# Optimization experiments

Measured on AMD Instinct MI355X. Metric: run time of the kernel, lower is better.

## Reference

```python
import jax, jax.numpy as jnp
import numpy as np

BATCH, SEQ, D_MODEL, D_STATE = 4, 2048, 512, 64
LN_EPS = 1e-5

def setup_inputs() -> dict:
    key = jax.random.key(0)
    ks = jax.random.split(key, 8)
    x = jax.random.normal(ks[0], (BATCH, SEQ, D_MODEL), jnp.float32)
    log_A_real = jax.random.normal(ks[1], (D_MODEL, D_STATE), jnp.float32)
    A_imag = jax.random.normal(ks[2], (D_MODEL, D_STATE), jnp.float32)
    B_param = jax.random.normal(ks[3], (D_MODEL, D_STATE, 2), jnp.float32) * 0.01
    C_param = jax.random.normal(ks[4], (D_MODEL, D_STATE, 2), jnp.float32) * 0.01
    D_param = jnp.ones((D_MODEL,), jnp.float32)
    W_out = jax.random.normal(ks[5], (D_MODEL, D_MODEL), jnp.float32) * (1.0 / np.sqrt(D_MODEL))
    b_out = jnp.zeros((D_MODEL,), jnp.float32)
    gamma = jnp.ones((D_MODEL,), jnp.float32)
    beta = jnp.zeros((D_MODEL,), jnp.float32)
    return dict(x=x, log_A_real=log_A_real, A_imag=A_imag, B_param=B_param,
                C_param=C_param, D_param=D_param, W_out=W_out, b_out=b_out,
                gamma=gamma, beta=beta)


def reference(x, log_A_real, A_imag, B_param, C_param, D_param, W_out, b_out, gamma, beta):
    Bn, L, d = x.shape
    # diagonal complex SSM parameters
    A = -jnp.exp(log_A_real) + 1j * A_imag                  # (d, s) complex, Re(A) < 0
    Bc = B_param[..., 0] + 1j * B_param[..., 1]              # (d, s)
    Cc = C_param[..., 0] + 1j * C_param[..., 1]              # (d, s)
    # kernel: K[d, l] = Re( sum_s conj(C) * exp(l*A) * B )
    powers = jnp.arange(L, dtype=jnp.float32)[:, None, None]  # (L,1,1)
    A_pow = jnp.exp(powers * A[None])                         # (L, d, s) complex
    CB = jnp.conj(Cc) * Bc                                    # (d, s)
    K = jnp.einsum('ds,lds->dl', CB, A_pow).real              # (d, L)
    # FFT convolution (matches torch flip + rfft conv + slice [L-1:2L-1])
    x_t = jnp.swapaxes(x, 1, 2)                               # (B, d, L)
    K_fl = jnp.flip(K, axis=-1)
    n = 2 * L
    Xf = jnp.fft.rfft(x_t, n=n, axis=-1)
    Kf = jnp.fft.rfft(K_fl, n=n, axis=-1)
    y = jnp.fft.irfft(Xf * Kf[None], n=n, axis=-1)[..., L - 1:2 * L - 1]
    y = y + D_param[None, :, None] * x_t                      # skip term D*x
    y = jnp.swapaxes(y, 1, 2)                                 # (B, L, d)
    y = y @ W_out.T + b_out                                   # out_proj (dropout p=0)
    z = y + x                                                 # residual
    mu = jnp.mean(z, axis=-1, keepdims=True)
    var = jnp.var(z, axis=-1, keepdims=True)
    return gamma * (z - mu) / jnp.sqrt(var + LN_EPS) + beta
```

## Files before the change

### kernel.cpp

```cpp
#include <hip/hip_runtime.h>
#include <hip/hip_bf16.h>
#include <stdint.h>
#include <stddef.h>

#define BATCH 4
#define SEQ   2048
#define DM    512
#define NST   64
#define LN_EPS 1e-5f
#define NCH   32
#define KDIM  192

typedef __attribute__((ext_vector_type(8))) short short8;
typedef __attribute__((ext_vector_type(4))) float f32x4;

__device__ __forceinline__ ushort f2bf(float f) {
    __hip_bfloat16 h = __float2bfloat16(f);
    return *(ushort*)&h;
}
__device__ __forceinline__ float bf2f(ushort u) {
    __hip_bfloat16 h = *(__hip_bfloat16*)&u;
    return __bfloat162float(h);
}

__global__ __launch_bounds__(256) void k_prep(
    const float* __restrict__ x, const float* __restrict__ W,
    __hip_bfloat16* __restrict__ xT, __hip_bfloat16* __restrict__ Wbf)
{
    __shared__ float smem[64][33];
    const int tid = threadIdx.x;
    const int bid = blockIdx.x;

    if (bid < 2048) {
        const int dt = bid & 15, lt = (bid >> 4) & 31, b = bid >> 9;
        const int l0 = lt * 64, d0 = dt * 32;
        const int dd = tid & 31, lr = tid >> 5;
        #pragma unroll
        for (int it = 0; it < 8; ++it) {
            int ll = it * 8 + lr;
            smem[ll][dd] = x[((size_t)b * SEQ + l0 + ll) * DM + d0 + dd];
        }
        __syncthreads();
        const int dw = tid >> 3, lg = (tid & 7) * 8;
        ushort pk[8];
        #pragma unroll
        for (int i = 0; i < 8; ++i) pk[i] = f2bf(smem[lg + i][dw]);
        *(short8*)&xT[((size_t)(d0 + dw) * BATCH + b) * SEQ + l0 + lg] = *(short8*)pk;
    } else {
        int i = (bid - 2048) * 256 + tid;
        if (i < DM * DM) Wbf[i] = __float2bfloat16(W[i]);
    }
}

__global__ __launch_bounds__(512) void k_ssm(
    const float* __restrict__ logA, const float* __restrict__ Aim,
    const float* __restrict__ Bp, const float* __restrict__ Cp,
    const __hip_bfloat16* __restrict__ xT, const float* __restrict__ Dp,
    __hip_bfloat16* __restrict__ yT)
{
    __shared__ short Zs[128 * 24 * 8];
    __shared__ __align__(16) char Rgn[128 * 129 * 4];
    __shared__ float Klds[64];
    __shared__ float2 e64s[64];
    short* Gs = (short*)Rgn;
    float (*Us)[129] = (float(*)[129])Rgn;
    short* Ms = (short*)Rgn;

    const int tid = threadIdx.x;
    const int d = blockIdx.x;
    const int w = tid >> 6, lane = tid & 63;
    const int q = lane >> 4, n = lane & 15;

    short8 xr[2];
    #pragma unroll
    for (int it = 0; it < 2; ++it) {
        int id = it * 512 + tid;
        int col = id >> 3, ck = id & 7;
        int bb = col >> 5, ch = col & 31;
        xr[it] = *(const short8*)&xT[((size_t)d * BATCH + bb) * SEQ + ch * 64 + ck * 8];
    }

    uint mca[8];
    {
        const int s = lane;
        const int i = d * NST + s;
        float aa  = expf(logA[i]);
        float wim = Aim[i];
        float mag = expf(-aa);
        float er = mag * cosf(wim), ei = mag * sinf(wim);
        float Br = Bp[2*i], Bi = Bp[2*i+1];
        float Cr = Cp[2*i], Ci = Cp[2*i+1];
        float CBr = Cr*Br + Ci*Bi;
        float CBi = Cr*Bi - Ci*Br;

        float e2r = er*er - ei*ei,   e2i = 2.f*er*ei;
        float e4r = e2r*e2r - e2i*e2i, e4i = 2.f*e2r*e2i;
        float e8r = e4r*e4r - e4i*e4i, e8i = 2.f*e4r*e4i;
        float ar, ai;
        if (w == 0)      { ar = 1.f;  ai = 0.f; }
        else if (w == 1) { ar = e8r;  ai = e8i; }
        else {
            float e16r = e8r*e8r - e8i*e8i, e16i = 2.f*e8r*e8i;
            if (w == 2)      { ar = e16r; ai = e16i; }
            else if (w == 3) { ar = e16r*e8r - e16i*e8i;  ai = e16r*e8i + e16i*e8r; }
            else {
                float e32r = e16r*e16r - e16i*e16i, e32i = 2.f*e16r*e16i;
                if (w == 4)      { ar = e32r; ai = e32i; }
                else if (w == 5) { ar = e32r*e8r - e32i*e8i;   ai = e32r*e8i + e32i*e8r; }
                else if (w == 6) { ar = e32r*e16r - e32i*e16i; ai = e32r*e16i + e32i*e16r; }
                else {
                    float e48r = e32r*e16r - e32i*e16i, e48i = e32r*e16i + e32i*e16r;
                    ar = e48r*e8r - e48i*e8i;  ai = e48r*e8i + e48i*e8r;
                }
            }
        }
        float prr = CBr*ar - CBi*ai;
        float pii = CBr*ai + CBi*ar;

        float kb[8];
        ushort gR[8], gI[8];
        #pragma unroll
        for (int tt = 0; tt < 8; ++tt) {
            kb[tt] = prr;
            gR[tt] = f2bf(prr);
            gI[tt] = f2bf(pii);
            float npr = er*prr - ei*pii, npi = er*pii + ei*prr;  prr = npr; pii = npi;
            float nar = er*ar - ei*ai,   nai = er*ai + ei*ar;    ar = nar; ai = nai;
            mca[tt] = (uint)f2bf(ar) | ((uint)f2bf(-ai) << 16);
        }
        if (w == 7) e64s[s] = make_float2(ar, ai);

        short8 v;
        int row = 2 * s;
        #pragma unroll
        for (int e = 0; e < 8; ++e) v[e] = (short)gR[e];
        { int cs = w ^ (row & 7); *(short8*)&Gs[(row * 8 + cs) * 8] = v; }
        row = 2 * s + 1;
        #pragma unroll
        for (int e = 0; e < 8; ++e) v[e] = (short)gI[e];
        { int cs = w ^ (row & 7); *(short8*)&Gs[(row * 8 + cs) * 8] = v; }

        #pragma unroll
        for (int tt = 0; tt < 8; ++tt) {
            float v2 = kb[tt];
            #pragma unroll
            for (int mask = 1; mask < 64; mask <<= 1) v2 += __shfl_xor(v2, mask);
            if (lane == 0) Klds[8 * w + tt] = v2;
        }
    }

    #pragma unroll
    for (int it = 0; it < 2; ++it) {
        int id = it * 512 + tid;
        int col = id >> 3, ck = id & 7;
        int cs = ck ^ (col & 7);
        *(short8*)&Zs[(col * 24 + cs) * 8] = xr[it];
    }
    __syncthreads();

    f32x4 acc1[8];
    {
        #pragma unroll
        for (int nf = 0; nf < 8; ++nf)
            #pragma unroll
            for (int k = 0; k < 4; ++k) acc1[nf][k] = 0.f;

        const int arow = w * 16 + n;
        #pragma unroll
        for (int kt = 0; kt < 2; ++kt) {
            int c = kt * 4 + q;
            int csa = c ^ (arow & 7);
            short8 af = *(const short8*)&Gs[(arow * 8 + csa) * 8];
            #pragma unroll
            for (int nf = 0; nf < 8; ++nf) {
                int col = nf * 16 + n;
                int csb = c ^ (col & 7);
                short8 bf = *(const short8*)&Zs[(col * 24 + csb) * 8];
                acc1[nf] = __builtin_amdgcn_mfma_f32_16x16x32_bf16(af, bf, acc1[nf], 0, 0, 0);
            }
        }
    }
    __syncthreads();

    {
        const int r0w = w * 16 + q * 4;
        #pragma unroll
        for (int nf = 0; nf < 8; ++nf) {
            int col = nf * 16 + n;
            #pragma unroll
            for (int r = 0; r < 4; ++r) Us[r0w + r][col] = acc1[nf][r];
        }
    }
    __syncthreads();

    if (tid < 256) {
        const int bb = tid >> 6, s = tid & 63;
        const int st = s >> 2, so = (s & 3) * 2;
        float2 a64 = e64s[s];
        const float er = a64.x, ei = a64.y;
        {
            int col = bb * 32 + 31;
            int c = 8 + st, cs = (c & ~7) | ((c & 7) ^ (col & 7));
            *(uint*)&Zs[(col * 24 + cs) * 8 + so] = 0u;
        }
        float gr = Us[2 * s][bb * 32 + 31], gi = Us[2 * s + 1][bb * 32 + 31];
        {
            int col = bb * 32 + 30;
            int c = 8 + st, cs = (c & ~7) | ((c & 7) ^ (col & 7));
            *(uint*)&Zs[(col * 24 + cs) * 8 + so] = (uint)f2bf(gr) | ((uint)f2bf(gi) << 16);
        }
        #pragma unroll 6
        for (int ch = 30; ch >= 1; --ch) {
            float ur = Us[2 * s][bb * 32 + ch], ui = Us[2 * s + 1][bb * 32 + ch];
            float nr = ur + er * gr - ei * gi;
            float ni = ui + er * gi + ei * gr;
            gr = nr; gi = ni;
            int col = bb * 32 + ch - 1;
            int c = 8 + st, cs = (c & ~7) | ((c & 7) ^ (col & 7));
            *(uint*)&Zs[(col * 24 + cs) * 8 + so] = (uint)f2bf(gr) | ((uint)f2bf(gi) << 16);
        }
    }
    __syncthreads();

    {
        {
            int id = tid;
            int row = id >> 3, c = id & 7;
            short8 v;
            #pragma unroll
            for (int e = 0; e < 8; ++e) {
                int col = c * 8 + e;
                float kv = (col >= row) ? Klds[col - row] : 0.f;
                v[e] = (short)f2bf(kv);
            }
            int cs = c ^ (row & 7);
            *(short8*)&Ms[(row * 24 + cs) * 8] = v;
        }
        const int s = lane;
        const int cc = 8 + (s >> 2);
        const int soff = 2 * (s & 3);
        #pragma unroll
        for (int tt = 0; tt < 8; ++tt) {
            int row = 63 - (8 * w + tt);
            int cs = (cc & ~7) | ((cc & 7) ^ (row & 7));
            *(uint*)&Ms[(row * 24 + cs) * 8 + soff] = mca[tt];
        }
    }
    __syncthreads();

    f32x4 acc[4];
    #pragma unroll
    for (int nf = 0; nf < 4; ++nf)
        #pragma unroll
        for (int k = 0; k < 4; ++k) acc[nf][k] = 0.f;

    const int arow = (w >> 1) * 16 + n;
    const int nfb  = (w & 1) * 4;
    #pragma unroll
    for (int kt = 0; kt < 6; ++kt) {
        int c = kt * 4 + q;
        int csa = (c & ~7) | ((c & 7) ^ (arow & 7));
        short8 af = *(const short8*)&Ms[(arow * 24 + csa) * 8];
        #pragma unroll
        for (int j = 0; j < 4; ++j) {
            int col = (nfb + j) * 16 + n;
            int csb = (c & ~7) | ((c & 7) ^ (col & 7));
            short8 bfr = *(const short8*)&Zs[(col * 24 + csb) * 8];
            acc[j] = __builtin_amdgcn_mfma_f32_16x16x32_bf16(af, bfr, acc[j], 0, 0, 0);
        }
    }

    const float Dd = Dp[d];
    const int i0 = (w >> 1) * 16 + q * 4;
    #pragma unroll
    for (int j = 0; j < 4; ++j) {
        int col = (nfb + j) * 16 + n;
        int bb = col >> 5, ch = col & 31;
        int cx = (i0 >> 3) ^ (col & 7);
        const ushort* zp = (const ushort*)&Zs[(col * 24 + cx) * 8 + (i0 & 7)];
        ushort o[4];
        #pragma unroll
        for (int r = 0; r < 4; ++r)
            o[r] = f2bf(acc[j][r] + Dd * bf2f(zp[r]));
        *(uint2*)&yT[((size_t)d * BATCH + bb) * SEQ + ch * 64 + i0] = *(uint2*)o;
    }
}

__global__ __launch_bounds__(512) void k_gemm_ln(
    const __hip_bfloat16* __restrict__ yT, const __hip_bfloat16* __restrict__ Wbf,
    const float* __restrict__ x, const float* __restrict__ bout,
    const float* __restrict__ gamma, const float* __restrict__ beta,
    float* __restrict__ out)
{
    __shared__ short Af[32][520];
    __shared__ short Bs[2][512][32];
    __shared__ float red[8][32][2];
    __shared__ float stats[32][2];

    const int tid  = threadIdx.x;
    const int w    = tid >> 6;
    const int lane = tid & 63;
    const int q    = lane >> 4;
    const int m    = lane & 15;
    const int r0   = blockIdx.x * 32;
    const int bq   = r0 >> 11;
    const int l0   = r0 & 2047;

    {
        const int kdb = tid >> 3, lg = (tid & 7) * 4;
        uint2 u[8];
        #pragma unroll
        for (int j = 0; j < 8; ++j)
            u[j] = *(const uint2*)&yT[((size_t)(j * 64 + kdb) * BATCH + bq) * SEQ + l0 + lg];
        #pragma unroll
        for (int j = 0; j < 8; ++j) {
            int kd = j * 64 + kdb;
            Af[lg + 0][kd] = (short)(u[j].x & 0xffff);
            Af[lg + 1][kd] = (short)(u[j].x >> 16);
            Af[lg + 2][kd] = (short)(u[j].y & 0xffff);
            Af[lg + 3][kd] = (short)(u[j].y >> 16);
        }
    }

    short8 nb0, nb1, nb2, nb3;
    const int ob = tid >> 2, jb = tid & 3;
    const int js = (jb ^ (ob & 3)) * 8;
    #define LOADB(k0) { \
        nb0 = *(const short8*)(Wbf + (size_t)(ob      ) * DM + (k0) + jb * 8); \
        nb1 = *(const short8*)(Wbf + (size_t)(ob + 128) * DM + (k0) + jb * 8); \
        nb2 = *(const short8*)(Wbf + (size_t)(ob + 256) * DM + (k0) + jb * 8); \
        nb3 = *(const short8*)(Wbf + (size_t)(ob + 384) * DM + (k0) + jb * 8); }
    #define WRITEB(p) { \
        *(short8*)&Bs[p][ob      ][js] = nb0; \
        *(short8*)&Bs[p][ob + 128][js] = nb1; \
        *(short8*)&Bs[p][ob + 256][js] = nb2; \
        *(short8*)&Bs[p][ob + 384][js] = nb3; }

    LOADB(0);
    WRITEB(0);
    LOADB(32);
    __syncthreads();

    f32x4 acc[2][4];
    #pragma unroll
    for (int a = 0; a < 2; ++a)
        #pragma unroll
        for (int nn = 0; nn < 4; ++nn)
            #pragma unroll
            for (int k = 0; k < 4; ++k) acc[a][nn][k] = 0.f;

    int p = 0;
    for (int k = 0; k < 16; ++k) {
        if (k < 15) WRITEB(p ^ 1);
        if (k < 14) LOADB((k + 2) * 32);
        const int k0 = k * 32;
        short8 a0 = *(const short8*)&Af[m][k0 + q * 8];
        short8 a1 = *(const short8*)&Af[16 + m][k0 + q * 8];
        #pragma unroll
        for (int nf = 0; nf < 4; ++nf) {
            int o = w * 64 + nf * 16 + m;
            short8 bb = *(const short8*)&Bs[p][o][(q ^ (m & 3)) * 8];
            acc[0][nf] = __builtin_amdgcn_mfma_f32_16x16x32_bf16(a0, bb, acc[0][nf], 0, 0, 0);
            acc[1][nf] = __builtin_amdgcn_mfma_f32_16x16x32_bf16(a1, bb, acc[1][nf], 0, 0, 0);
        }
        __syncthreads();
        p ^= 1;
    }
    #undef LOADB
    #undef WRITEB

    float bo[4], ga[4], be[4];
    #pragma unroll
    for (int nf = 0; nf < 4; ++nf) {
        int o = w * 64 + nf * 16 + m;
        bo[nf] = bout[o]; ga[nf] = gamma[o]; be[nf] = beta[o];
    }

    float rs[2][4], rq[2][4];
    #pragma unroll
    for (int mf = 0; mf < 2; ++mf)
        #pragma unroll
        for (int i = 0; i < 4; ++i) { rs[mf][i] = 0.f; rq[mf][i] = 0.f; }

    #pragma unroll
    for (int mf = 0; mf < 2; ++mf)
        #pragma unroll
        for (int nf = 0; nf < 4; ++nf) {
            int o = w * 64 + nf * 16 + m;
            #pragma unroll
            for (int i = 0; i < 4; ++i) {
                int row = mf * 16 + q * 4 + i;
                float zv = acc[mf][nf][i] + bo[nf] + x[(size_t)(r0 + row) * DM + o];
                acc[mf][nf][i] = zv;
                rs[mf][i] += zv;
                rq[mf][i] += zv * zv;
            }
        }

    #pragma unroll
    for (int mask = 1; mask < 16; mask <<= 1) {
        #pragma unroll
        for (int mf = 0; mf < 2; ++mf)
            #pragma unroll
            for (int i = 0; i < 4; ++i) {
                rs[mf][i] += __shfl_xor(rs[mf][i], mask);
                rq[mf][i] += __shfl_xor(rq[mf][i], mask);
            }
    }
    if (m == 0) {
        #pragma unroll
        for (int mf = 0; mf < 2; ++mf)
            #pragma unroll
            for (int i = 0; i < 4; ++i) {
                int row = mf * 16 + q * 4 + i;
                red[w][row][0] = rs[mf][i];
                red[w][row][1] = rq[mf][i];
            }
    }
    __syncthreads();
    if (tid < 32) {
        float s = 0.f, sq = 0.f;
        #pragma unroll
        for (int ww = 0; ww < 8; ++ww) { s += red[ww][tid][0]; sq += red[ww][tid][1]; }
        float mu  = s * (1.f / DM);
        float var = sq * (1.f / DM) - mu * mu;
        stats[tid][0] = mu;
        stats[tid][1] = 1.f / sqrtf(var + LN_EPS);
    }
    __syncthreads();

    #pragma unroll
    for (int mf = 0; mf < 2; ++mf)
        #pragma unroll
        for (int i = 0; i < 4; ++i) {
            int row = mf * 16 + q * 4 + i;
            float mu = stats[row][0], rstd = stats[row][1];
            #pragma unroll
            for (int nf = 0; nf < 4; ++nf) {
                int o = w * 64 + nf * 16 + m;
                out[(size_t)(r0 + row) * DM + o] =
                    ga[nf] * (acc[mf][nf][i] - mu) * rstd + be[nf];
            }
        }
}

extern "C" void kernel_launch(void* const* d_in, const int* in_sizes, int n_in,
                              void* d_out, int out_size, void* d_ws, size_t ws_size,
                              hipStream_t stream)
{
    const float* x    = (const float*)d_in[0];
    const float* logA = (const float*)d_in[1];
    const float* Aim  = (const float*)d_in[2];
    const float* Bp   = (const float*)d_in[3];
    const float* Cp   = (const float*)d_in[4];
    const float* Dp   = (const float*)d_in[5];
    const float* W    = (const float*)d_in[6];
    const float* bo   = (const float*)d_in[7];
    const float* ga   = (const float*)d_in[8];
    const float* be   = (const float*)d_in[9];

    char* ws = (char*)d_ws;
    __hip_bfloat16* Wbf = (__hip_bfloat16*)ws;
    __hip_bfloat16* xT  = (__hip_bfloat16*)(ws + (3u << 20));
    __hip_bfloat16* yT  = (__hip_bfloat16*)(ws + (41u << 20));

    k_prep   <<<3072, 256, 0, stream>>>(x, W, xT, Wbf);
    k_ssm    <<<DM, 512, 0, stream>>>(logA, Aim, Bp, Cp, xT, Dp, yT);
    k_gemm_ln<<<(BATCH * SEQ) / 32, 512, 0, stream>>>(yT, Wbf, x, bo, ga, be, (float*)d_out);
}
```

Before: 48.43 us.

## Split SSM kernel across batch halves to double block count

Each k_ssm block now handles one channel and two of the four batches, so the grid grows from 512 to 1024 blocks. Per-block shared memory shrinks, since Zs and Us are halved and Us moves to a separate region after the G/M area. The goal is more parallelism and occupancy on the many CUs of the GPU. The cost is that each block repeats the per-channel setup work (exp/sin/cos, kernel powers, the G and M matrices), which is now done twice per channel.

```diff
diff --git a/kernel.cpp b/kernel.cpp
--- a/kernel.cpp
+++ b/kernel.cpp
@@ -58,26 +58,25 @@
     const __hip_bfloat16* __restrict__ xT, const float* __restrict__ Dp,
     __hip_bfloat16* __restrict__ yT)
 {
-    __shared__ short Zs[128 * 24 * 8];
-    __shared__ __align__(16) char Rgn[128 * 129 * 4];
+    __shared__ short Zs[64 * 24 * 8];
+    __shared__ __align__(16) char Rgn[16384 + 128 * 65 * 4];
     __shared__ float Klds[64];
     __shared__ float2 e64s[64];
     short* Gs = (short*)Rgn;
-    float (*Us)[129] = (float(*)[129])Rgn;
+    float (*Us)[65] = (float(*)[65])(Rgn + 16384);
     short* Ms = (short*)Rgn;
 
     const int tid = threadIdx.x;
-    const int d = blockIdx.x;
+    const int d    = blockIdx.x >> 1;
+    const int bb0  = (blockIdx.x & 1) * 2;
     const int w = tid >> 6, lane = tid & 63;
     const int q = lane >> 4, n = lane & 15;
 
-    short8 xr[2];
-    #pragma unroll
-    for (int it = 0; it < 2; ++it) {
-        int id = it * 512 + tid;
-        int col = id >> 3, ck = id & 7;
-        int bb = col >> 5, ch = col & 31;
-        xr[it] = *(const short8*)&xT[((size_t)d * BATCH + bb) * SEQ + ch * 64 + ck * 8];
+    short8 xr;
+    {
+        int col = tid >> 3, ck = tid & 7;
+        int b = bb0 + (col >> 5), ch = col & 31;
+        xr = *(const short8*)&xT[((size_t)d * BATCH + b) * SEQ + ch * 64 + ck * 8];
     }
 
     uint mca[8];
@@ -149,19 +148,17 @@
         }
     }
 
-    #pragma unroll
-    for (int it = 0; it < 2; ++it) {
-        int id = it * 512 + tid;
-        int col = id >> 3, ck = id & 7;
+    {
+        int col = tid >> 3, ck = tid & 7;
         int cs = ck ^ (col & 7);
-        *(short8*)&Zs[(col * 24 + cs) * 8] = xr[it];
-    }
-    __syncthreads();
-
-    f32x4 acc1[8];
-    {
-        #pragma unroll
-        for (int nf = 0; nf < 8; ++nf)
+        *(short8*)&Zs[(col * 24 + cs) * 8] = xr;
+    }
+    __syncthreads();
+
+    f32x4 acc1[4];
+    {
+        #pragma unroll
+        for (int nf = 0; nf < 4; ++nf)
             #pragma unroll
             for (int k = 0; k < 4; ++k) acc1[nf][k] = 0.f;
 
@@ -172,7 +169,7 @@
             int csa = c ^ (arow & 7);
             short8 af = *(const short8*)&Gs[(arow * 8 + csa) * 8];
             #pragma unroll
-            for (int nf = 0; nf < 8; ++nf) {
+            for (int nf = 0; nf < 4; ++nf) {
                 int col = nf * 16 + n;
                 int csb = c ^ (col & 7);
                 short8 bf = *(const short8*)&Zs[(col * 24 + csb) * 8];
@@ -185,7 +182,7 @@
     {
         const int r0w = w * 16 + q * 4;
         #pragma unroll
-        for (int nf = 0; nf < 8; ++nf) {
+        for (int nf = 0; nf < 4; ++nf) {
             int col = nf * 16 + n;
             #pragma unroll
             for (int r = 0; r < 4; ++r) Us[r0w + r][col] = acc1[nf][r];
@@ -193,29 +190,29 @@
     }
     __syncthreads();
 
-    if (tid < 256) {
-        const int bb = tid >> 6, s = tid & 63;
+    if (tid < 128) {
+        const int bl = tid >> 6, s = tid & 63;
         const int st = s >> 2, so = (s & 3) * 2;
         float2 a64 = e64s[s];
         const float er = a64.x, ei = a64.y;
         {
-            int col = bb * 32 + 31;
+            int col = bl * 32 + 31;
             int c = 8 + st, cs = (c & ~7) | ((c & 7) ^ (col & 7));
             *(uint*)&Zs[(col * 24 + cs) * 8 + so] = 0u;
         }
-        float gr = Us[2 * s][bb * 32 + 31], gi = Us[2 * s + 1][bb * 32 + 31];
+        float gr = Us[2 * s][bl * 32 + 31], gi = Us[2 * s + 1][bl * 32 + 31];
         {
-            int col = bb * 32 + 30;
+            int col = bl * 32 + 30;
             int c = 8 + st, cs = (c & ~7) | ((c & 7) ^ (col & 7));
             *(uint*)&Zs[(col * 24 + cs) * 8 + so] = (uint)f2bf(gr) | ((uint)f2bf(gi) << 16);
         }
         #pragma unroll 6
         for (int ch = 30; ch >= 1; --ch) {
-            float ur = Us[2 * s][bb * 32 + ch], ui = Us[2 * s + 1][bb * 32 + ch];
+            float ur = Us[2 * s][bl * 32 + ch], ui = Us[2 * s + 1][bl * 32 + ch];
             float nr = ur + er * gr - ei * gi;
             float ni = ui + er * gi + ei * gr;
             gr = nr; gi = ni;
-            int col = bb * 32 + ch - 1;
+            int col = bl * 32 + ch - 1;
             int c = 8 + st, cs = (c & ~7) | ((c & 7) ^ (col & 7));
             *(uint*)&Zs[(col * 24 + cs) * 8 + so] = (uint)f2bf(gr) | ((uint)f2bf(gi) << 16);
         }
@@ -248,22 +245,22 @@
     }
     __syncthreads();
 
-    f32x4 acc[4];
-    #pragma unroll
-    for (int nf = 0; nf < 4; ++nf)
-        #pragma unroll
-        for (int k = 0; k < 4; ++k) acc[nf][k] = 0.f;
+    f32x4 acc[2];
+    #pragma unroll
+    for (int j = 0; j < 2; ++j)
+        #pragma unroll
+        for (int k = 0; k < 4; ++k) acc[j][k] = 0.f;
 
     const int arow = (w >> 1) * 16 + n;
-    const int nfb  = (w & 1) * 4;
+    const int jfb  = (w & 1) * 2;
     #pragma unroll
     for (int kt = 0; kt < 6; ++kt) {
         int c = kt * 4 + q;
         int csa = (c & ~7) | ((c & 7) ^ (arow & 7));
         short8 af = *(const short8*)&Ms[(arow * 24 + csa) * 8];
         #pragma unroll
-        for (int j = 0; j < 4; ++j) {
-            int col = (nfb + j) * 16 + n;
+        for (int j = 0; j < 2; ++j) {
+            int col = (jfb + j) * 16 + n;
             int csb = (c & ~7) | ((c & 7) ^ (col & 7));
             short8 bfr = *(const short8*)&Zs[(col * 24 + csb) * 8];
             acc[j] = __builtin_amdgcn_mfma_f32_16x16x32_bf16(af, bfr, acc[j], 0, 0, 0);
@@ -273,16 +270,16 @@
     const float Dd = Dp[d];
     const int i0 = (w >> 1) * 16 + q * 4;
     #pragma unroll
-    for (int j = 0; j < 4; ++j) {
-        int col = (nfb + j) * 16 + n;
-        int bb = col >> 5, ch = col & 31;
+    for (int j = 0; j < 2; ++j) {
+        int col = (jfb + j) * 16 + n;
+        int b = bb0 + (col >> 5), ch = col & 31;
         int cx = (i0 >> 3) ^ (col & 7);
         const ushort* zp = (const ushort*)&Zs[(col * 24 + cx) * 8 + (i0 & 7)];
         ushort o[4];
         #pragma unroll
         for (int r = 0; r < 4; ++r)
             o[r] = f2bf(acc[j][r] + Dd * bf2f(zp[r]));
-        *(uint2*)&yT[((size_t)d * BATCH + bb) * SEQ + ch * 64 + i0] = *(uint2*)o;
+        *(uint2*)&yT[((size_t)d * BATCH + b) * SEQ + ch * 64 + i0] = *(uint2*)o;
     }
 }
 
@@ -465,6 +462,6 @@
     __hip_bfloat16* yT  = (__hip_bfloat16*)(ws + (41u << 20));
 
     k_prep   <<<3072, 256, 0, stream>>>(x, W, xT, Wbf);
-    k_ssm    <<<DM, 512, 0, stream>>>(logA, Aim, Bp, Cp, xT, Dp, yT);
+    k_ssm    <<<DM * 2, 512, 0, stream>>>(logA, Aim, Bp, Cp, xT, Dp, yT);
     k_gemm_ln<<<(BATCH * SEQ) / 32, 512, 0, stream>>>(yT, Wbf, x, bo, ga, be, (float*)d_out);
 }
```

After: 48.64 us. Within noise of the previous version (+0.4%).
